# Kernel tuning notes

Hardware: AMD Instinct MI355X
Metric: run time of the kernel (lower is better)

## Reference

```python
import jax, jax.numpy as jnp
import numpy as np

EPS = 1e-5


def conv2d(x, w, b, stride=1, pad=1):
    out = jax.lax.conv_general_dilated(
        x, w, (stride, stride), [(pad, pad), (pad, pad)],
        dimension_numbers=('NCHW', 'OIHW', 'NCHW'))
    return out + b[None, :, None, None]


def bn_inf(x, gamma, beta, mean, var):
    inv = gamma / jnp.sqrt(var + EPS)
    return x * inv[None, :, None, None] + (beta - mean * inv)[None, :, None, None]


def deform_conv(x, offset, weight, stride, pad, dil):
    # x: [B,Ci,H,W], offset: [B,2*K*K,Ho,Wo] (dy,dx interleaved per kernel pos),
    # weight: [Co,Ci,K,K]. torchvision DeformConv2d v1 semantics, no bias.
    B, Ci, H, W = x.shape
    Co, _, K, _ = weight.shape
    KK = K * K
    Ho = (H + 2 * pad - dil * (K - 1) - 1) // stride + 1
    Wo = (W + 2 * pad - dil * (K - 1) - 1) // stride + 1
    dy = offset[:, 0::2]  # [B,KK,Ho,Wo]
    dx = offset[:, 1::2]
    ky, kx = jnp.meshgrid(jnp.arange(K), jnp.arange(K), indexing='ij')
    ky = ky.reshape(KK).astype(x.dtype)
    kx = kx.reshape(KK).astype(x.dtype)
    base_y = (jnp.arange(Ho) * stride - pad).astype(x.dtype)
    base_x = (jnp.arange(Wo) * stride - pad).astype(x.dtype)
    ys = base_y[None, None, :, None] + (ky * dil)[None, :, None, None] + dy
    xs = base_x[None, None, None, :] + (kx * dil)[None, :, None, None] + dx
    y0 = jnp.floor(ys)
    x0 = jnp.floor(xs)
    fy = ys - y0
    fx = xs - x0

    def gather(img, iy, ix):
        # img: [Ci,H,W]; iy, ix: [KK,Ho,Wo] float integer-valued coords
        valid = (iy >= 0) & (iy < H) & (ix >= 0) & (ix < W)
        iyc = jnp.clip(iy, 0, H - 1).astype(jnp.int32)
        ixc = jnp.clip(ix, 0, W - 1).astype(jnp.int32)
        v = img[:, iyc, ixc]  # [Ci,KK,Ho,Wo]
        return v * valid[None].astype(img.dtype)

    def sample_one(img, y0b, x0b, fyb, fxb):
        w00 = (1 - fyb) * (1 - fxb)
        w01 = (1 - fyb) * fxb
        w10 = fyb * (1 - fxb)
        w11 = fyb * fxb
        s = (gather(img, y0b, x0b) * w00[None]
             + gather(img, y0b, x0b + 1) * w01[None]
             + gather(img, y0b + 1, x0b) * w10[None]
             + gather(img, y0b + 1, x0b + 1) * w11[None])
        return s  # [Ci,KK,Ho,Wo]

    sampled = jax.vmap(sample_one)(x, y0, x0, fy, fx)  # [B,Ci,KK,Ho,Wo]
    return jnp.einsum('oik,bikhw->bohw', weight.reshape(Co, Ci, KK), sampled)


def setup_inputs() -> dict:
    key = jax.random.key(0)
    ks = jax.random.split(key, 16)
    B, C, H, W = 8, 128, 64, 64
    d = dict(
        x=jax.random.normal(ks[0], (B, C, H, W), jnp.float32),
        w_off1=jax.random.normal(ks[1], (18, C, 3, 3), jnp.float32) * 0.01,
        b_off1=jnp.zeros((18,), jnp.float32),
        w_dc1=jax.random.normal(ks[2], (C, C, 3, 3), jnp.float32) * 0.05,
        g1=jnp.ones((C,), jnp.float32),
        beta1=jnp.zeros((C,), jnp.float32),
        m1=jax.random.normal(ks[3], (C,), jnp.float32) * 0.1,
        v1=jax.random.uniform(ks[4], (C,), jnp.float32) + 0.5,
        w_off2=jax.random.normal(ks[5], (18, C, 3, 3), jnp.float32) * 0.01,
        b_off2=jnp.zeros((18,), jnp.float32),
        w_dc2=jax.random.normal(ks[6], (C, C, 3, 3), jnp.float32) * 0.05,
        g2=jnp.ones((C,), jnp.float32),
        beta2=jnp.zeros((C,), jnp.float32),
        m2=jax.random.normal(ks[7], (C,), jnp.float32) * 0.1,
        v2=jax.random.uniform(ks[8], (C,), jnp.float32) + 0.5,
    )
    return d


def reference(x, w_off1, b_off1, w_dc1, g1, beta1, m1, v1,
              w_off2, b_off2, w_dc2, g2, beta2, m2, v2):
    # BasicBlock6 forward (stride=1, in_planes==planes => identity shortcut)
    off1 = conv2d(x, w_off1, b_off1, stride=1, pad=1)
    out = jax.nn.relu(bn_inf(deform_conv(x, off1, w_dc1, 1, 2, 2), g1, beta1, m1, v1))
    off2 = conv2d(out, w_off2, b_off2, stride=1, pad=1)
    out = bn_inf(deform_conv(out, off2, w_dc2, 1, 2, 2), g2, beta2, m2, v2)
    out = out + x  # identity shortcut
    return jax.nn.relu(out)
```

## Files before the change

### kernel.cpp

```cpp
#include <hip/hip_runtime.h>
#include <hip/hip_bf16.h>

#define CH   128
#define HH   64
#define WW   64
#define OFFC 18

typedef __attribute__((ext_vector_type(8))) short bf16x8;
typedef __attribute__((ext_vector_type(4))) short bf16x4;
typedef __attribute__((ext_vector_type(4))) float f32x4;

static __device__ __forceinline__ unsigned short f2bf(float f) {
    __hip_bfloat16 h = __float2bfloat16(f);
    return *reinterpret_cast<unsigned short*>(&h);
}
static __device__ __forceinline__ float bf2f(unsigned short u) {
    union { unsigned int i; float f; } x; x.i = ((unsigned int)u) << 16;
    return x.f;
}

__global__ __launch_bounds__(256) void pack_all_kernel(
    const float* __restrict__ wdc1, const float* __restrict__ wdc2,
    const float* __restrict__ wof1, const float* __restrict__ wof2,
    unsigned short* __restrict__ wpk1, unsigned short* __restrict__ wpk2,
    unsigned short* __restrict__ wpo1, unsigned short* __restrict__ wpo2)
{
    int blk = blockIdx.x;
    int tid = threadIdx.x;
    if (blk < 1152) {
        const float* w = (blk < 576) ? wdc1 : wdc2;
        unsigned short* wp = (blk < 576) ? wpk1 : wpk2;
        int id = (blk % 576) * 256 + tid;
        int j    = id & 7;
        int lane = (id >> 3) & 63;
        int ot   = (id >> 9) & 7;
        int kk   = (id >> 12) & 3;
        int k    = id >> 14;
        int o = ot * 16 + (lane & 15);
        int i = kk * 32 + (lane >> 4) * 8 + j;
        wp[id] = f2bf(w[(o * CH + i) * 9 + k]);
    } else {
        const float* w = (blk < 1296) ? wof1 : wof2;
        unsigned short* wp = (blk < 1296) ? wpo1 : wpo2;
        int id = ((blk - 1152) % 144) * 256 + tid;
        int j    = id & 7;
        int lane = (id >> 3) & 63;
        int mt   = (id >> 9) & 1;
        int kk   = (id >> 10) & 3;
        int k    = id >> 12;
        int o = mt * 16 + (lane & 15);
        int i = kk * 32 + (lane >> 4) * 8 + j;
        wp[id] = (o < OFFC) ? f2bf(w[(o * CH + i) * 9 + k]) : (unsigned short)0;
    }
}

__global__ __launch_bounds__(256) void to_nhwc_kernel(
    const float* __restrict__ x, unsigned short* __restrict__ xh)
{
    __shared__ float s[CH][WW + 1];
    int blk = blockIdx.x;
    int tid = threadIdx.x;
    const float* xb = x + ((size_t)(blk >> 6) * CH * HH + (blk & 63)) * WW;

    int c_off = tid >> 4, w0 = (tid & 15) * 4;
    #pragma unroll
    for (int it = 0; it < 8; ++it) {
        int c = it * 16 + c_off;
        float4 vv = *(const float4*)&xb[(size_t)c * HH * WW + w0];
        s[c][w0] = vv.x; s[c][w0 + 1] = vv.y; s[c][w0 + 2] = vv.z; s[c][w0 + 3] = vv.w;
    }
    __syncthreads();

    int w = tid & 63, c0 = (tid >> 6) * 32;
    unsigned short* dst = xh + ((size_t)blk * WW + w) * CH + c0;
    unsigned short tmp[32];
    #pragma unroll
    for (int j = 0; j < 32; ++j) tmp[j] = f2bf(s[c0 + j][w]);
    #pragma unroll
    for (int q = 0; q < 4; ++q)
        *(bf16x8*)(dst + q * 8) = *(const bf16x8*)(tmp + q * 8);
}

__global__ __launch_bounds__(256) void off_conv_mfma_kernel(
    const unsigned short* __restrict__ xh,
    const unsigned short* __restrict__ wpo,
    const float* __restrict__ bias,
    unsigned short* __restrict__ offh)
{
    int wgid = blockIdx.x;
    int blk  = (wgid & 7) * 64 + (wgid >> 3);
    int b = blk >> 6, oh = blk & 63;
    int tid = threadIdx.x;
    int lane = tid & 63;
    int nt = tid >> 6;
    int nl = lane & 15;
    int kg = lane >> 4;

    f32x4 acc0 = {0.f, 0.f, 0.f, 0.f}, acc1 = {0.f, 0.f, 0.f, 0.f};
    const unsigned short* xb = xh + (size_t)b * HH * WW * CH;

    for (int k = 0; k < 9; ++k) {
        int ky = k / 3, kx = k - ky * 3;
        int ih = oh - 1 + ky;
        if (ih < 0 || ih >= HH) continue;
        int iw = nt * 16 + nl + kx - 1;
        bool valid = (iw >= 0) && (iw < WW);
        const unsigned short* row = xb + ((size_t)ih * WW + (valid ? iw : 0)) * CH + kg * 8;
        const unsigned short* wk = wpo + (size_t)k * 8 * 512;
        #pragma unroll
        for (int kk = 0; kk < 4; ++kk) {
            bf16x8 bfrag = {0, 0, 0, 0, 0, 0, 0, 0};
            if (valid) bfrag = *(const bf16x8*)(row + kk * 32);
            bf16x8 a0 = *(const bf16x8*)(wk + (kk * 2 + 0) * 512 + lane * 8);
            bf16x8 a1 = *(const bf16x8*)(wk + (kk * 2 + 1) * 512 + lane * 8);
            acc0 = __builtin_amdgcn_mfma_f32_16x16x32_bf16(a0, bfrag, acc0, 0, 0, 0);
            acc1 = __builtin_amdgcn_mfma_f32_16x16x32_bf16(a1, bfrag, acc1, 0, 0, 0);
        }
    }

    int ow = nt * 16 + nl;
    #pragma unroll
    for (int r = 0; r < 4; ++r) {
        int co = kg * 4 + r;
        offh[(((size_t)b * OFFC + co) * HH + oh) * WW + ow] = f2bf(acc0[r] + bias[co]);
    }
    if (kg == 0) {
        #pragma unroll
        for (int r = 0; r < 2; ++r) {
            int co = 16 + r;
            offh[(((size_t)b * OFFC + co) * HH + oh) * WW + ow] = f2bf(acc1[r] + bias[co]);
        }
    }
}

__global__ __launch_bounds__(256) void deform_mfma2_kernel(
    const unsigned short* __restrict__ xh,
    const unsigned short* __restrict__ offh,
    const unsigned short* __restrict__ wpk,
    const float* __restrict__ g, const float* __restrict__ beta,
    const float* __restrict__ m, const float* __restrict__ v,
    const float* __restrict__ residual,
    unsigned short* __restrict__ out_h,
    float* __restrict__ out_f)
{
    __shared__ unsigned short sB[32 * 128];

    int wgid = blockIdx.x;
    int blk  = (wgid & 7) * 128 + (wgid >> 3);
    int owh = blk & 1, oh = (blk >> 1) & 63, b = blk >> 7;
    int ow0 = owh * 32;
    int tid = threadIdx.x, lane = tid & 63, wv = tid >> 6;

    int s_ow = tid >> 3;
    int ci0  = (tid & 7) * 16;
    int ow_g = ow0 + s_ow;

    const unsigned short* xb = xh + (size_t)b * HH * WW * CH;

    f32x4 acc[2][2];
    #pragma unroll
    for (int a = 0; a < 2; ++a)
        #pragma unroll
        for (int q = 0; q < 2; ++q) acc[a][q] = (f32x4){0.f, 0.f, 0.f, 0.f};

    for (int k = 0; k < 9; ++k) {
        int ky = k / 3, kx = k - ky * 3;

        float dy = bf2f(offh[(((size_t)b * OFFC + 2 * k) * HH + oh) * WW + ow_g]);
        float dx = bf2f(offh[(((size_t)b * OFFC + 2 * k + 1) * HH + oh) * WW + ow_g]);
        float ys = (float)(oh - 2 + ky * 2) + dy;
        float xs = (float)(ow_g - 2 + kx * 2) + dx;
        float y0f = floorf(ys), x0f = floorf(xs);
        float fy = ys - y0f, fx = xs - x0f;
        int y0 = (int)y0f, x0 = (int)x0f;
        int y1 = y0 + 1,   x1 = x0 + 1;
        bool vy0 = (y0 >= 0) & (y0 < HH);
        bool vy1 = (y1 >= 0) & (y1 < HH);
        bool vx0 = (x0 >= 0) & (x0 < WW);
        bool vx1 = (x1 >= 0) & (x1 < WW);
        int y0c = min(max(y0, 0), HH - 1), y1c = min(max(y1, 0), HH - 1);
        int x0c = min(max(x0, 0), WW - 1), x1c = min(max(x1, 0), WW - 1);
        float cw0 = (1.f - fy) * (1.f - fx) * ((vy0 && vx0) ? 1.f : 0.f);
        float cw1 = (1.f - fy) * fx         * ((vy0 && vx1) ? 1.f : 0.f);
        float cw2 = fy * (1.f - fx)         * ((vy1 && vx0) ? 1.f : 0.f);
        float cw3 = fy * fx                 * ((vy1 && vx1) ? 1.f : 0.f);

        const unsigned short* p0 = xb + ((size_t)(y0c * WW + x0c)) * CH + ci0;
        const unsigned short* p1 = xb + ((size_t)(y0c * WW + x1c)) * CH + ci0;
        const unsigned short* p2 = xb + ((size_t)(y1c * WW + x0c)) * CH + ci0;
        const unsigned short* p3 = xb + ((size_t)(y1c * WW + x1c)) * CH + ci0;

        bf16x8 v00 = *(const bf16x8*)(p0),     v01 = *(const bf16x8*)(p0 + 8);
        bf16x8 v10 = *(const bf16x8*)(p1),     v11 = *(const bf16x8*)(p1 + 8);
        bf16x8 v20 = *(const bf16x8*)(p2),     v21 = *(const bf16x8*)(p2 + 8);
        bf16x8 v30 = *(const bf16x8*)(p3),     v31 = *(const bf16x8*)(p3 + 8);

        union { bf16x8 v8; unsigned short u[8]; } w0, w1;
        #pragma unroll
        for (int j = 0; j < 8; ++j) {
            float a0 = cw0 * bf2f((unsigned short)v00[j])
                     + cw1 * bf2f((unsigned short)v10[j])
                     + cw2 * bf2f((unsigned short)v20[j])
                     + cw3 * bf2f((unsigned short)v30[j]);
            float a1 = cw0 * bf2f((unsigned short)v01[j])
                     + cw1 * bf2f((unsigned short)v11[j])
                     + cw2 * bf2f((unsigned short)v21[j])
                     + cw3 * bf2f((unsigned short)v31[j]);
            w0.u[j] = f2bf(a0);
            w1.u[j] = f2bf(a1);
        }
        int base = s_ow * 256 + ci0 * 2;
        int swz  = (s_ow & 7) << 4;
        *(bf16x8*)((char*)sB + ( base       ^ swz)) = w0.v8;
        *(bf16x8*)((char*)sB + ((base + 16) ^ swz)) = w1.v8;
        __syncthreads();

        const unsigned short* wk = wpk + (size_t)k * 16384;
        #pragma unroll
        for (int kk = 0; kk < 4; ++kk) {
            bf16x8 a0 = *(const bf16x8*)(wk + (kk * 8 + 2 * wv)     * 512 + lane * 8);
            bf16x8 a1 = *(const bf16x8*)(wk + (kk * 8 + 2 * wv + 1) * 512 + lane * 8);
            #pragma unroll
            for (int owt = 0; owt < 2; ++owt) {
                int owl = owt * 16 + (lane & 15);
                int rbyte = (owl * 256 + (kk * 32 + (lane >> 4) * 8) * 2)
                            ^ ((owl & 7) << 4);
                bf16x8 bf = *(const bf16x8*)((const char*)sB + rbyte);
                acc[0][owt] = __builtin_amdgcn_mfma_f32_16x16x32_bf16(
                                  a0, bf, acc[0][owt], 0, 0, 0);
                acc[1][owt] = __builtin_amdgcn_mfma_f32_16x16x32_bf16(
                                  a1, bf, acc[1][owt], 0, 0, 0);
            }
        }
        __syncthreads();
    }

    if (out_h != nullptr) {
        #pragma unroll
        for (int otl = 0; otl < 2; ++otl) {
            int ob = (2 * wv + otl) * 16 + (lane >> 4) * 4;
            float inv[4], sh[4];
            #pragma unroll
            for (int r = 0; r < 4; ++r) {
                int o = ob + r;
                float iv = g[o] / sqrtf(v[o] + 1e-5f);
                inv[r] = iv; sh[r] = beta[o] - m[o] * iv;
            }
            #pragma unroll
            for (int owt = 0; owt < 2; ++owt) {
                int ow = ow0 + owt * 16 + (lane & 15);
                union { bf16x4 v4; unsigned short u[4]; } pk;
                #pragma unroll
                for (int r = 0; r < 4; ++r) {
                    float val = acc[otl][owt][r] * inv[r] + sh[r];
                    pk.u[r] = f2bf(fmaxf(val, 0.f));
                }
                *(bf16x4*)(out_h + ((size_t)(b * HH + oh) * WW + ow) * CH + ob) = pk.v4;
            }
        }
    } else {
        #pragma unroll
        for (int otl = 0; otl < 2; ++otl) {
            #pragma unroll
            for (int r = 0; r < 4; ++r) {
                int o = (2 * wv + otl) * 16 + (lane >> 4) * 4 + r;
                float iv = g[o] / sqrtf(v[o] + 1e-5f);
                float sh = beta[o] - m[o] * iv;
                #pragma unroll
                for (int owt = 0; owt < 2; ++owt) {
                    int ow = ow0 + owt * 16 + (lane & 15);
                    size_t idx = (((size_t)b * CH + o) * HH + oh) * WW + ow;
                    float val = acc[otl][owt][r] * iv + sh + residual[idx];
                    out_f[idx] = fmaxf(val, 0.f);
                }
            }
        }
    }
}

extern "C" void kernel_launch(void* const* d_in, const int* in_sizes, int n_in,
                              void* d_out, int out_size, void* d_ws, size_t ws_size,
                              hipStream_t stream)
{
    const float* x      = (const float*)d_in[0];
    const float* w_off1 = (const float*)d_in[1];
    const float* b_off1 = (const float*)d_in[2];
    const float* w_dc1  = (const float*)d_in[3];
    const float* g1     = (const float*)d_in[4];
    const float* beta1  = (const float*)d_in[5];
    const float* m1     = (const float*)d_in[6];
    const float* v1     = (const float*)d_in[7];
    const float* w_off2 = (const float*)d_in[8];
    const float* b_off2 = (const float*)d_in[9];
    const float* w_dc2  = (const float*)d_in[10];
    const float* g2     = (const float*)d_in[11];
    const float* beta2  = (const float*)d_in[12];
    const float* m2     = (const float*)d_in[13];
    const float* v2     = (const float*)d_in[14];
    float* out = (float*)d_out;

    char* ws = (char*)d_ws;
    unsigned short* xh    = (unsigned short*)ws;
    unsigned short* out1h = (unsigned short*)(ws + 8388608);
    unsigned short* offh  = (unsigned short*)(ws + 16777216);
    unsigned short* wpk1  = (unsigned short*)(ws + 17956864);
    unsigned short* wpk2  = (unsigned short*)(ws + 18251776);
    unsigned short* wpo1  = (unsigned short*)(ws + 18546688);
    unsigned short* wpo2  = (unsigned short*)(ws + 18620416);

    pack_all_kernel<<<1440, 256, 0, stream>>>(w_dc1, w_dc2, w_off1, w_off2,
                                              wpk1, wpk2, wpo1, wpo2);
    to_nhwc_kernel<<<512, 256, 0, stream>>>(x, xh);

    off_conv_mfma_kernel<<<512, 256, 0, stream>>>(xh, wpo1, b_off1, offh);
    deform_mfma2_kernel<<<1024, 256, 0, stream>>>(xh, offh, wpk1,
                                                  g1, beta1, m1, v1,
                                                  nullptr, out1h, nullptr);
    off_conv_mfma_kernel<<<512, 256, 0, stream>>>(out1h, wpo2, b_off2, offh);
    deform_mfma2_kernel<<<1024, 256, 0, stream>>>(out1h, offh, wpk2,
                                                  g2, beta2, m2, v2,
                                                  x, nullptr, out);
}
```

Before: 101.5 us.

## Double-buffer deform sampling with MFMA and merge prep kernels into one launch

The deform kernel now double-buffers its shared-memory sample tile. Gathers for the next kernel tap are issued before the MFMAs for the current tap, so global-load latency can hide behind matrix math. All 18 offsets are loaded up front, and one barrier per tap is removed. The weight-packing and NHWC conversion kernels are merged into a single launch to save launch overhead, at the cost of doubled LDS and higher register pressure in the deform kernel.

```diff
diff --git a/kernel.cpp b/kernel.cpp
--- a/kernel.cpp
+++ b/kernel.cpp
@@ -19,14 +19,17 @@
     return x.f;
 }
 
-__global__ __launch_bounds__(256) void pack_all_kernel(
+__global__ __launch_bounds__(256) void prep_kernel(
+    const float* __restrict__ x, unsigned short* __restrict__ xh,
     const float* __restrict__ wdc1, const float* __restrict__ wdc2,
     const float* __restrict__ wof1, const float* __restrict__ wof2,
     unsigned short* __restrict__ wpk1, unsigned short* __restrict__ wpk2,
     unsigned short* __restrict__ wpo1, unsigned short* __restrict__ wpo2)
 {
+    __shared__ float s[CH][WW + 1];
     int blk = blockIdx.x;
     int tid = threadIdx.x;
+
     if (blk < 1152) {
         const float* w = (blk < 576) ? wdc1 : wdc2;
         unsigned short* wp = (blk < 576) ? wpk1 : wpk2;
@@ -39,7 +42,9 @@
         int o = ot * 16 + (lane & 15);
         int i = kk * 32 + (lane >> 4) * 8 + j;
         wp[id] = f2bf(w[(o * CH + i) * 9 + k]);
-    } else {
+        return;
+    }
+    if (blk < 1440) {
         const float* w = (blk < 1296) ? wof1 : wof2;
         unsigned short* wp = (blk < 1296) ? wpo1 : wpo2;
         int id = ((blk - 1152) % 144) * 256 + tid;
@@ -51,16 +56,11 @@
         int o = mt * 16 + (lane & 15);
         int i = kk * 32 + (lane >> 4) * 8 + j;
         wp[id] = (o < OFFC) ? f2bf(w[(o * CH + i) * 9 + k]) : (unsigned short)0;
-    }
-}
-
-__global__ __launch_bounds__(256) void to_nhwc_kernel(
-    const float* __restrict__ x, unsigned short* __restrict__ xh)
-{
-    __shared__ float s[CH][WW + 1];
-    int blk = blockIdx.x;
-    int tid = threadIdx.x;
-    const float* xb = x + ((size_t)(blk >> 6) * CH * HH + (blk & 63)) * WW;
+        return;
+    }
+
+    int nb = blk - 1440;
+    const float* xb = x + ((size_t)(nb >> 6) * CH * HH + (nb & 63)) * WW;
 
     int c_off = tid >> 4, w0 = (tid & 15) * 4;
     #pragma unroll
@@ -72,7 +72,7 @@
     __syncthreads();
 
     int w = tid & 63, c0 = (tid >> 6) * 32;
-    unsigned short* dst = xh + ((size_t)blk * WW + w) * CH + c0;
+    unsigned short* dst = xh + ((size_t)nb * WW + w) * CH + c0;
     unsigned short tmp[32];
     #pragma unroll
     for (int j = 0; j < 32; ++j) tmp[j] = f2bf(s[c0 + j][w]);
@@ -133,6 +133,75 @@
     }
 }
 
+#define DEF_COORD(K) do {                                                     \
+    int ky = (K) / 3, kx = (K) - ky * 3;                                      \
+    float ys = (float)(oh - 2 + ky * 2) + dyv[K];                             \
+    float xs = (float)(ow_g - 2 + kx * 2) + dxv[K];                           \
+    float y0f = floorf(ys), x0f = floorf(xs);                                 \
+    float fy = ys - y0f, fx = xs - x0f;                                       \
+    int y0 = (int)y0f, x0i = (int)x0f;                                        \
+    int y1 = y0 + 1, x1 = x0i + 1;                                            \
+    bool vy0 = (y0 >= 0) & (y0 < HH), vy1 = (y1 >= 0) & (y1 < HH);            \
+    bool vx0 = (x0i >= 0) & (x0i < WW), vx1 = (x1 >= 0) & (x1 < WW);          \
+    int y0c = min(max(y0, 0), HH - 1), y1c = min(max(y1, 0), HH - 1);         \
+    int x0c = min(max(x0i, 0), WW - 1), x1c = min(max(x1, 0), WW - 1);        \
+    cw0 = (1.f - fy) * (1.f - fx) * ((vy0 && vx0) ? 1.f : 0.f);               \
+    cw1 = (1.f - fy) * fx         * ((vy0 && vx1) ? 1.f : 0.f);               \
+    cw2 = fy * (1.f - fx)         * ((vy1 && vx0) ? 1.f : 0.f);               \
+    cw3 = fy * fx                 * ((vy1 && vx1) ? 1.f : 0.f);               \
+    p0 = xb + ((size_t)(y0c * WW + x0c)) * CH + ci0;                          \
+    p1 = xb + ((size_t)(y0c * WW + x1c)) * CH + ci0;                          \
+    p2 = xb + ((size_t)(y1c * WW + x0c)) * CH + ci0;                          \
+    p3 = xb + ((size_t)(y1c * WW + x1c)) * CH + ci0;                          \
+} while (0)
+
+#define DEF_LOADS() do {                                                      \
+    s0a = *(const bf16x8*)(p0); s0b = *(const bf16x8*)(p0 + 8);               \
+    s1a = *(const bf16x8*)(p1); s1b = *(const bf16x8*)(p1 + 8);               \
+    s2a = *(const bf16x8*)(p2); s2b = *(const bf16x8*)(p2 + 8);               \
+    s3a = *(const bf16x8*)(p3); s3b = *(const bf16x8*)(p3 + 8);               \
+} while (0)
+
+#define DEF_BLEND_WRITE(BUF) do {                                             \
+    union { bf16x8 v8; unsigned short u[8]; } w0u, w1u;                       \
+    _Pragma("unroll")                                                         \
+    for (int j = 0; j < 8; ++j) {                                             \
+        float a0 = cw0 * bf2f((unsigned short)s0a[j])                         \
+                 + cw1 * bf2f((unsigned short)s1a[j])                         \
+                 + cw2 * bf2f((unsigned short)s2a[j])                         \
+                 + cw3 * bf2f((unsigned short)s3a[j]);                        \
+        float a1 = cw0 * bf2f((unsigned short)s0b[j])                         \
+                 + cw1 * bf2f((unsigned short)s1b[j])                         \
+                 + cw2 * bf2f((unsigned short)s2b[j])                         \
+                 + cw3 * bf2f((unsigned short)s3b[j]);                        \
+        w0u.u[j] = f2bf(a0); w1u.u[j] = f2bf(a1);                             \
+    }                                                                         \
+    int base = s_ow * 256 + ci0 * 2;                                          \
+    int swz  = (s_ow & 7) << 4;                                               \
+    *(bf16x8*)((char*)sB[BUF] + ( base        ^ swz)) = w0u.v8;               \
+    *(bf16x8*)((char*)sB[BUF] + ((base + 16)  ^ swz)) = w1u.v8;               \
+} while (0)
+
+#define DEF_MFMA(K, BUF) do {                                                 \
+    const unsigned short* wk = wpk + (size_t)(K) * 16384;                     \
+    _Pragma("unroll")                                                         \
+    for (int kk = 0; kk < 4; ++kk) {                                          \
+        bf16x8 a0 = *(const bf16x8*)(wk + (kk * 8 + 2 * wv)     * 512 + lane * 8); \
+        bf16x8 a1 = *(const bf16x8*)(wk + (kk * 8 + 2 * wv + 1) * 512 + lane * 8); \
+        _Pragma("unroll")                                                     \
+        for (int owt = 0; owt < 2; ++owt) {                                   \
+            int owl = owt * 16 + (lane & 15);                                 \
+            int rbyte = (owl * 256 + (kk * 32 + (lane >> 4) * 8) * 2)         \
+                        ^ ((owl & 7) << 4);                                   \
+            bf16x8 bfv = *(const bf16x8*)((const char*)sB[BUF] + rbyte);      \
+            acc[0][owt] = __builtin_amdgcn_mfma_f32_16x16x32_bf16(            \
+                              a0, bfv, acc[0][owt], 0, 0, 0);                 \
+            acc[1][owt] = __builtin_amdgcn_mfma_f32_16x16x32_bf16(            \
+                              a1, bfv, acc[1][owt], 0, 0, 0);                 \
+        }                                                                     \
+    }                                                                         \
+} while (0)
+
 __global__ __launch_bounds__(256) void deform_mfma2_kernel(
     const unsigned short* __restrict__ xh,
     const unsigned short* __restrict__ offh,
@@ -143,7 +212,7 @@
     unsigned short* __restrict__ out_h,
     float* __restrict__ out_f)
 {
-    __shared__ unsigned short sB[32 * 128];
+    __shared__ unsigned short sB[2][32 * 128];
 
     int wgid = blockIdx.x;
     int blk  = (wgid & 7) * 128 + (wgid >> 3);
@@ -157,81 +226,31 @@
 
     const unsigned short* xb = xh + (size_t)b * HH * WW * CH;
 
+    float dyv[9], dxv[9];
+    #pragma unroll
+    for (int k = 0; k < 9; ++k) {
+        dyv[k] = bf2f(offh[(((size_t)b * OFFC + 2 * k)     * HH + oh) * WW + ow_g]);
+        dxv[k] = bf2f(offh[(((size_t)b * OFFC + 2 * k + 1) * HH + oh) * WW + ow_g]);
+    }
+
     f32x4 acc[2][2];
     #pragma unroll
     for (int a = 0; a < 2; ++a)
         #pragma unroll
         for (int q = 0; q < 2; ++q) acc[a][q] = (f32x4){0.f, 0.f, 0.f, 0.f};
 
+    float cw0, cw1, cw2, cw3;
+    const unsigned short *p0, *p1, *p2, *p3;
+    bf16x8 s0a, s0b, s1a, s1b, s2a, s2b, s3a, s3b;
+
+    DEF_COORD(0); DEF_LOADS(); DEF_BLEND_WRITE(0);
+    __syncthreads();
+
+    #pragma unroll
     for (int k = 0; k < 9; ++k) {
-        int ky = k / 3, kx = k - ky * 3;
-
-        float dy = bf2f(offh[(((size_t)b * OFFC + 2 * k) * HH + oh) * WW + ow_g]);
-        float dx = bf2f(offh[(((size_t)b * OFFC + 2 * k + 1) * HH + oh) * WW + ow_g]);
-        float ys = (float)(oh - 2 + ky * 2) + dy;
-        float xs = (float)(ow_g - 2 + kx * 2) + dx;
-        float y0f = floorf(ys), x0f = floorf(xs);
-        float fy = ys - y0f, fx = xs - x0f;
-        int y0 = (int)y0f, x0 = (int)x0f;
-        int y1 = y0 + 1,   x1 = x0 + 1;
-        bool vy0 = (y0 >= 0) & (y0 < HH);
-        bool vy1 = (y1 >= 0) & (y1 < HH);
-        bool vx0 = (x0 >= 0) & (x0 < WW);
-        bool vx1 = (x1 >= 0) & (x1 < WW);
-        int y0c = min(max(y0, 0), HH - 1), y1c = min(max(y1, 0), HH - 1);
-        int x0c = min(max(x0, 0), WW - 1), x1c = min(max(x1, 0), WW - 1);
-        float cw0 = (1.f - fy) * (1.f - fx) * ((vy0 && vx0) ? 1.f : 0.f);
-        float cw1 = (1.f - fy) * fx         * ((vy0 && vx1) ? 1.f : 0.f);
-        float cw2 = fy * (1.f - fx)         * ((vy1 && vx0) ? 1.f : 0.f);
-        float cw3 = fy * fx                 * ((vy1 && vx1) ? 1.f : 0.f);
-
-        const unsigned short* p0 = xb + ((size_t)(y0c * WW + x0c)) * CH + ci0;
-        const unsigned short* p1 = xb + ((size_t)(y0c * WW + x1c)) * CH + ci0;
-        const unsigned short* p2 = xb + ((size_t)(y1c * WW + x0c)) * CH + ci0;
-        const unsigned short* p3 = xb + ((size_t)(y1c * WW + x1c)) * CH + ci0;
-
-        bf16x8 v00 = *(const bf16x8*)(p0),     v01 = *(const bf16x8*)(p0 + 8);
-        bf16x8 v10 = *(const bf16x8*)(p1),     v11 = *(const bf16x8*)(p1 + 8);
-        bf16x8 v20 = *(const bf16x8*)(p2),     v21 = *(const bf16x8*)(p2 + 8);
-        bf16x8 v30 = *(const bf16x8*)(p3),     v31 = *(const bf16x8*)(p3 + 8);
-
-        union { bf16x8 v8; unsigned short u[8]; } w0, w1;
-        #pragma unroll
-        for (int j = 0; j < 8; ++j) {
-            float a0 = cw0 * bf2f((unsigned short)v00[j])
-                     + cw1 * bf2f((unsigned short)v10[j])
-                     + cw2 * bf2f((unsigned short)v20[j])
-                     + cw3 * bf2f((unsigned short)v30[j]);
-            float a1 = cw0 * bf2f((unsigned short)v01[j])
-                     + cw1 * bf2f((unsigned short)v11[j])
-                     + cw2 * bf2f((unsigned short)v21[j])
-                     + cw3 * bf2f((unsigned short)v31[j]);
-            w0.u[j] = f2bf(a0);
-            w1.u[j] = f2bf(a1);
-        }
-        int base = s_ow * 256 + ci0 * 2;
-        int swz  = (s_ow & 7) << 4;
-        *(bf16x8*)((char*)sB + ( base       ^ swz)) = w0.v8;
-        *(bf16x8*)((char*)sB + ((base + 16) ^ swz)) = w1.v8;
-        __syncthreads();
-
-        const unsigned short* wk = wpk + (size_t)k * 16384;
-        #pragma unroll
-        for (int kk = 0; kk < 4; ++kk) {
-            bf16x8 a0 = *(const bf16x8*)(wk + (kk * 8 + 2 * wv)     * 512 + lane * 8);
-            bf16x8 a1 = *(const bf16x8*)(wk + (kk * 8 + 2 * wv + 1) * 512 + lane * 8);
-            #pragma unroll
-            for (int owt = 0; owt < 2; ++owt) {
-                int owl = owt * 16 + (lane & 15);
-                int rbyte = (owl * 256 + (kk * 32 + (lane >> 4) * 8) * 2)
-                            ^ ((owl & 7) << 4);
-                bf16x8 bf = *(const bf16x8*)((const char*)sB + rbyte);
-                acc[0][owt] = __builtin_amdgcn_mfma_f32_16x16x32_bf16(
-                                  a0, bf, acc[0][owt], 0, 0, 0);
-                acc[1][owt] = __builtin_amdgcn_mfma_f32_16x16x32_bf16(
-                                  a1, bf, acc[1][owt], 0, 0, 0);
-            }
-        }
+        if (k < 8) { DEF_COORD(k + 1); DEF_LOADS(); }
+        DEF_MFMA(k, k & 1);
+        if (k < 8) DEF_BLEND_WRITE((k + 1) & 1);
         __syncthreads();
     }
 
@@ -308,9 +327,8 @@
     unsigned short* wpo1  = (unsigned short*)(ws + 18546688);
     unsigned short* wpo2  = (unsigned short*)(ws + 18620416);
 
-    pack_all_kernel<<<1440, 256, 0, stream>>>(w_dc1, w_dc2, w_off1, w_off2,
-                                              wpk1, wpk2, wpo1, wpo2);
-    to_nhwc_kernel<<<512, 256, 0, stream>>>(x, xh);
+    prep_kernel<<<1952, 256, 0, stream>>>(x, xh, w_dc1, w_dc2, w_off1, w_off2,
+                                          wpk1, wpk2, wpo1, wpo2);
 
     off_conv_mfma_kernel<<<512, 256, 0, stream>>>(xh, wpo1, b_off1, offh);
     deform_mfma2_kernel<<<1024, 256, 0, stream>>>(xh, offh, wpk1,
```

Measured after the change: 102.8 us. No clear change (+1.3%).

## Fuse offset conv into deformable conv kernel and merge prep kernels

Applied to the files above, without the earlier changes.

Computes the 18-channel offset convolution inside the deformable conv block, keeping the offsets in LDS as fp32 instead of writing them to global memory as bf16. Each block now covers a full 64-wide output row instead of half a row, and the weight packing and NHWC conversion are merged into a single prep kernel. This cuts the launch count from six to three and removes the offset buffer round trip. In exchange there are half as many blocks (512), more accumulators per thread, more LDS per block, and a serial offset-conv phase before sampling in each block.

```diff
diff --git a/kernel.cpp b/kernel.cpp
--- a/kernel.cpp
+++ b/kernel.cpp
@@ -19,14 +19,17 @@
     return x.f;
 }
 
-__global__ __launch_bounds__(256) void pack_all_kernel(
+__global__ __launch_bounds__(256) void prep_kernel(
+    const float* __restrict__ x, unsigned short* __restrict__ xh,
     const float* __restrict__ wdc1, const float* __restrict__ wdc2,
     const float* __restrict__ wof1, const float* __restrict__ wof2,
     unsigned short* __restrict__ wpk1, unsigned short* __restrict__ wpk2,
     unsigned short* __restrict__ wpo1, unsigned short* __restrict__ wpo2)
 {
+    __shared__ float s[CH][WW + 1];
     int blk = blockIdx.x;
     int tid = threadIdx.x;
+
     if (blk < 1152) {
         const float* w = (blk < 576) ? wdc1 : wdc2;
         unsigned short* wp = (blk < 576) ? wpk1 : wpk2;
@@ -39,7 +42,9 @@
         int o = ot * 16 + (lane & 15);
         int i = kk * 32 + (lane >> 4) * 8 + j;
         wp[id] = f2bf(w[(o * CH + i) * 9 + k]);
-    } else {
+        return;
+    }
+    if (blk < 1440) {
         const float* w = (blk < 1296) ? wof1 : wof2;
         unsigned short* wp = (blk < 1296) ? wpo1 : wpo2;
         int id = ((blk - 1152) % 144) * 256 + tid;
@@ -51,16 +56,11 @@
         int o = mt * 16 + (lane & 15);
         int i = kk * 32 + (lane >> 4) * 8 + j;
         wp[id] = (o < OFFC) ? f2bf(w[(o * CH + i) * 9 + k]) : (unsigned short)0;
-    }
-}
-
-__global__ __launch_bounds__(256) void to_nhwc_kernel(
-    const float* __restrict__ x, unsigned short* __restrict__ xh)
-{
-    __shared__ float s[CH][WW + 1];
-    int blk = blockIdx.x;
-    int tid = threadIdx.x;
-    const float* xb = x + ((size_t)(blk >> 6) * CH * HH + (blk & 63)) * WW;
+        return;
+    }
+
+    int nb = blk - 1440;
+    const float* xb = x + ((size_t)(nb >> 6) * CH * HH + (nb & 63)) * WW;
 
     int c_off = tid >> 4, w0 = (tid & 15) * 4;
     #pragma unroll
@@ -72,7 +72,7 @@
     __syncthreads();
 
     int w = tid & 63, c0 = (tid >> 6) * 32;
-    unsigned short* dst = xh + ((size_t)blk * WW + w) * CH + c0;
+    unsigned short* dst = xh + ((size_t)nb * WW + w) * CH + c0;
     unsigned short tmp[32];
     #pragma unroll
     for (int j = 0; j < 32; ++j) tmp[j] = f2bf(s[c0 + j][w]);
@@ -81,61 +81,10 @@
         *(bf16x8*)(dst + q * 8) = *(const bf16x8*)(tmp + q * 8);
 }
 
-__global__ __launch_bounds__(256) void off_conv_mfma_kernel(
+__global__ __launch_bounds__(256) void deform_fused_kernel(
     const unsigned short* __restrict__ xh,
     const unsigned short* __restrict__ wpo,
     const float* __restrict__ bias,
-    unsigned short* __restrict__ offh)
-{
-    int wgid = blockIdx.x;
-    int blk  = (wgid & 7) * 64 + (wgid >> 3);
-    int b = blk >> 6, oh = blk & 63;
-    int tid = threadIdx.x;
-    int lane = tid & 63;
-    int nt = tid >> 6;
-    int nl = lane & 15;
-    int kg = lane >> 4;
-
-    f32x4 acc0 = {0.f, 0.f, 0.f, 0.f}, acc1 = {0.f, 0.f, 0.f, 0.f};
-    const unsigned short* xb = xh + (size_t)b * HH * WW * CH;
-
-    for (int k = 0; k < 9; ++k) {
-        int ky = k / 3, kx = k - ky * 3;
-        int ih = oh - 1 + ky;
-        if (ih < 0 || ih >= HH) continue;
-        int iw = nt * 16 + nl + kx - 1;
-        bool valid = (iw >= 0) && (iw < WW);
-        const unsigned short* row = xb + ((size_t)ih * WW + (valid ? iw : 0)) * CH + kg * 8;
-        const unsigned short* wk = wpo + (size_t)k * 8 * 512;
-        #pragma unroll
-        for (int kk = 0; kk < 4; ++kk) {
-            bf16x8 bfrag = {0, 0, 0, 0, 0, 0, 0, 0};
-            if (valid) bfrag = *(const bf16x8*)(row + kk * 32);
-            bf16x8 a0 = *(const bf16x8*)(wk + (kk * 2 + 0) * 512 + lane * 8);
-            bf16x8 a1 = *(const bf16x8*)(wk + (kk * 2 + 1) * 512 + lane * 8);
-            acc0 = __builtin_amdgcn_mfma_f32_16x16x32_bf16(a0, bfrag, acc0, 0, 0, 0);
-            acc1 = __builtin_amdgcn_mfma_f32_16x16x32_bf16(a1, bfrag, acc1, 0, 0, 0);
-        }
-    }
-
-    int ow = nt * 16 + nl;
-    #pragma unroll
-    for (int r = 0; r < 4; ++r) {
-        int co = kg * 4 + r;
-        offh[(((size_t)b * OFFC + co) * HH + oh) * WW + ow] = f2bf(acc0[r] + bias[co]);
-    }
-    if (kg == 0) {
-        #pragma unroll
-        for (int r = 0; r < 2; ++r) {
-            int co = 16 + r;
-            offh[(((size_t)b * OFFC + co) * HH + oh) * WW + ow] = f2bf(acc1[r] + bias[co]);
-        }
-    }
-}
-
-__global__ __launch_bounds__(256) void deform_mfma2_kernel(
-    const unsigned short* __restrict__ xh,
-    const unsigned short* __restrict__ offh,
     const unsigned short* __restrict__ wpk,
     const float* __restrict__ g, const float* __restrict__ beta,
     const float* __restrict__ m, const float* __restrict__ v,
@@ -143,43 +92,77 @@
     unsigned short* __restrict__ out_h,
     float* __restrict__ out_f)
 {
-    __shared__ unsigned short sB[32 * 128];
+    __shared__ unsigned short sB[64 * 128];
+    __shared__ float off_lds[OFFC][WW];
 
     int wgid = blockIdx.x;
-    int blk  = (wgid & 7) * 128 + (wgid >> 3);
-    int owh = blk & 1, oh = (blk >> 1) & 63, b = blk >> 7;
-    int ow0 = owh * 32;
+    int blk  = (wgid & 7) * 64 + (wgid >> 3);
+    int b = blk >> 6, oh = blk & 63;
     int tid = threadIdx.x, lane = tid & 63, wv = tid >> 6;
 
-    int s_ow = tid >> 3;
-    int ci0  = (tid & 7) * 16;
-    int ow_g = ow0 + s_ow;
-
     const unsigned short* xb = xh + (size_t)b * HH * WW * CH;
 
-    f32x4 acc[2][2];
+    {
+        f32x4 oacc0 = {0.f, 0.f, 0.f, 0.f}, oacc1 = {0.f, 0.f, 0.f, 0.f};
+        for (int k = 0; k < 9; ++k) {
+            int ky = k / 3, kx = k - ky * 3;
+            int ih = oh - 1 + ky;
+            if (ih < 0 || ih >= HH) continue;
+            int iw = wv * 16 + (lane & 15) + kx - 1;
+            bool valid = (iw >= 0) && (iw < WW);
+            const unsigned short* row =
+                xb + ((size_t)ih * WW + (valid ? iw : 0)) * CH + (lane >> 4) * 8;
+            const unsigned short* wk = wpo + (size_t)k * 4096;
+            #pragma unroll
+            for (int kk = 0; kk < 4; ++kk) {
+                bf16x8 bfrag = {0, 0, 0, 0, 0, 0, 0, 0};
+                if (valid) bfrag = *(const bf16x8*)(row + kk * 32);
+                bf16x8 a0 = *(const bf16x8*)(wk + (kk * 2 + 0) * 512 + lane * 8);
+                bf16x8 a1 = *(const bf16x8*)(wk + (kk * 2 + 1) * 512 + lane * 8);
+                oacc0 = __builtin_amdgcn_mfma_f32_16x16x32_bf16(a0, bfrag, oacc0, 0, 0, 0);
+                oacc1 = __builtin_amdgcn_mfma_f32_16x16x32_bf16(a1, bfrag, oacc1, 0, 0, 0);
+            }
+        }
+        int ow = wv * 16 + (lane & 15);
+        #pragma unroll
+        for (int r = 0; r < 4; ++r) {
+            int co = (lane >> 4) * 4 + r;
+            off_lds[co][ow] = oacc0[r] + bias[co];
+        }
+        if ((lane >> 4) == 0) {
+            #pragma unroll
+            for (int r = 0; r < 2; ++r) {
+                int co = 16 + r;
+                off_lds[co][ow] = oacc1[r] + bias[co];
+            }
+        }
+    }
+    __syncthreads();
+
+    int s_ow = tid & 63;
+    int ci0  = (tid >> 6) * 32;
+
+    f32x4 acc[2][4];
     #pragma unroll
     for (int a = 0; a < 2; ++a)
         #pragma unroll
-        for (int q = 0; q < 2; ++q) acc[a][q] = (f32x4){0.f, 0.f, 0.f, 0.f};
+        for (int q = 0; q < 4; ++q) acc[a][q] = (f32x4){0.f, 0.f, 0.f, 0.f};
 
     for (int k = 0; k < 9; ++k) {
         int ky = k / 3, kx = k - ky * 3;
 
-        float dy = bf2f(offh[(((size_t)b * OFFC + 2 * k) * HH + oh) * WW + ow_g]);
-        float dx = bf2f(offh[(((size_t)b * OFFC + 2 * k + 1) * HH + oh) * WW + ow_g]);
+        float dy = off_lds[2 * k][s_ow];
+        float dx = off_lds[2 * k + 1][s_ow];
         float ys = (float)(oh - 2 + ky * 2) + dy;
-        float xs = (float)(ow_g - 2 + kx * 2) + dx;
+        float xs = (float)(s_ow - 2 + kx * 2) + dx;
         float y0f = floorf(ys), x0f = floorf(xs);
         float fy = ys - y0f, fx = xs - x0f;
-        int y0 = (int)y0f, x0 = (int)x0f;
-        int y1 = y0 + 1,   x1 = x0 + 1;
-        bool vy0 = (y0 >= 0) & (y0 < HH);
-        bool vy1 = (y1 >= 0) & (y1 < HH);
-        bool vx0 = (x0 >= 0) & (x0 < WW);
-        bool vx1 = (x1 >= 0) & (x1 < WW);
+        int y0 = (int)y0f, x0i = (int)x0f;
+        int y1 = y0 + 1, x1 = x0i + 1;
+        bool vy0 = (y0 >= 0) & (y0 < HH), vy1 = (y1 >= 0) & (y1 < HH);
+        bool vx0 = (x0i >= 0) & (x0i < WW), vx1 = (x1 >= 0) & (x1 < WW);
         int y0c = min(max(y0, 0), HH - 1), y1c = min(max(y1, 0), HH - 1);
-        int x0c = min(max(x0, 0), WW - 1), x1c = min(max(x1, 0), WW - 1);
+        int x0c = min(max(x0i, 0), WW - 1), x1c = min(max(x1, 0), WW - 1);
         float cw0 = (1.f - fy) * (1.f - fx) * ((vy0 && vx0) ? 1.f : 0.f);
         float cw1 = (1.f - fy) * fx         * ((vy0 && vx1) ? 1.f : 0.f);
         float cw2 = fy * (1.f - fx)         * ((vy1 && vx0) ? 1.f : 0.f);
@@ -190,29 +173,30 @@
         const unsigned short* p2 = xb + ((size_t)(y1c * WW + x0c)) * CH + ci0;
         const unsigned short* p3 = xb + ((size_t)(y1c * WW + x1c)) * CH + ci0;
 
-        bf16x8 v00 = *(const bf16x8*)(p0),     v01 = *(const bf16x8*)(p0 + 8);
-        bf16x8 v10 = *(const bf16x8*)(p1),     v11 = *(const bf16x8*)(p1 + 8);
-        bf16x8 v20 = *(const bf16x8*)(p2),     v21 = *(const bf16x8*)(p2 + 8);
-        bf16x8 v30 = *(const bf16x8*)(p3),     v31 = *(const bf16x8*)(p3 + 8);
-
-        union { bf16x8 v8; unsigned short u[8]; } w0, w1;
-        #pragma unroll
-        for (int j = 0; j < 8; ++j) {
-            float a0 = cw0 * bf2f((unsigned short)v00[j])
-                     + cw1 * bf2f((unsigned short)v10[j])
-                     + cw2 * bf2f((unsigned short)v20[j])
-                     + cw3 * bf2f((unsigned short)v30[j]);
-            float a1 = cw0 * bf2f((unsigned short)v01[j])
-                     + cw1 * bf2f((unsigned short)v11[j])
-                     + cw2 * bf2f((unsigned short)v21[j])
-                     + cw3 * bf2f((unsigned short)v31[j]);
-            w0.u[j] = f2bf(a0);
-            w1.u[j] = f2bf(a1);
-        }
         int base = s_ow * 256 + ci0 * 2;
         int swz  = (s_ow & 7) << 4;
-        *(bf16x8*)((char*)sB + ( base       ^ swz)) = w0.v8;
-        *(bf16x8*)((char*)sB + ((base + 16) ^ swz)) = w1.v8;
+        #pragma unroll
+        for (int q = 0; q < 2; ++q) {
+            bf16x8 v0a = *(const bf16x8*)(p0 + q * 16), v0b = *(const bf16x8*)(p0 + q * 16 + 8);
+            bf16x8 v1a = *(const bf16x8*)(p1 + q * 16), v1b = *(const bf16x8*)(p1 + q * 16 + 8);
+            bf16x8 v2a = *(const bf16x8*)(p2 + q * 16), v2b = *(const bf16x8*)(p2 + q * 16 + 8);
+            bf16x8 v3a = *(const bf16x8*)(p3 + q * 16), v3b = *(const bf16x8*)(p3 + q * 16 + 8);
+            union { bf16x8 v8; unsigned short u[8]; } wa, wb;
+            #pragma unroll
+            for (int j = 0; j < 8; ++j) {
+                float a0 = cw0 * bf2f((unsigned short)v0a[j])
+                         + cw1 * bf2f((unsigned short)v1a[j])
+                         + cw2 * bf2f((unsigned short)v2a[j])
+                         + cw3 * bf2f((unsigned short)v3a[j]);
+                float a1 = cw0 * bf2f((unsigned short)v0b[j])
+                         + cw1 * bf2f((unsigned short)v1b[j])
+                         + cw2 * bf2f((unsigned short)v2b[j])
+                         + cw3 * bf2f((unsigned short)v3b[j]);
+                wa.u[j] = f2bf(a0); wb.u[j] = f2bf(a1);
+            }
+            *(bf16x8*)((char*)sB + ((base + q * 32)      ^ swz)) = wa.v8;
+            *(bf16x8*)((char*)sB + ((base + q * 32 + 16) ^ swz)) = wb.v8;
+        }
         __syncthreads();
 
         const unsigned short* wk = wpk + (size_t)k * 16384;
@@ -221,15 +205,15 @@
             bf16x8 a0 = *(const bf16x8*)(wk + (kk * 8 + 2 * wv)     * 512 + lane * 8);
             bf16x8 a1 = *(const bf16x8*)(wk + (kk * 8 + 2 * wv + 1) * 512 + lane * 8);
             #pragma unroll
-            for (int owt = 0; owt < 2; ++owt) {
+            for (int owt = 0; owt < 4; ++owt) {
                 int owl = owt * 16 + (lane & 15);
                 int rbyte = (owl * 256 + (kk * 32 + (lane >> 4) * 8) * 2)
                             ^ ((owl & 7) << 4);
-                bf16x8 bf = *(const bf16x8*)((const char*)sB + rbyte);
+                bf16x8 bfv = *(const bf16x8*)((const char*)sB + rbyte);
                 acc[0][owt] = __builtin_amdgcn_mfma_f32_16x16x32_bf16(
-                                  a0, bf, acc[0][owt], 0, 0, 0);
+                                  a0, bfv, acc[0][owt], 0, 0, 0);
                 acc[1][owt] = __builtin_amdgcn_mfma_f32_16x16x32_bf16(
-                                  a1, bf, acc[1][owt], 0, 0, 0);
+                                  a1, bfv, acc[1][owt], 0, 0, 0);
             }
         }
         __syncthreads();
@@ -247,8 +231,8 @@
                 inv[r] = iv; sh[r] = beta[o] - m[o] * iv;
             }
             #pragma unroll
-            for (int owt = 0; owt < 2; ++owt) {
-                int ow = ow0 + owt * 16 + (lane & 15);
+            for (int owt = 0; owt < 4; ++owt) {
+                int ow = owt * 16 + (lane & 15);
                 union { bf16x4 v4; unsigned short u[4]; } pk;
                 #pragma unroll
                 for (int r = 0; r < 4; ++r) {
@@ -267,8 +251,8 @@
                 float iv = g[o] / sqrtf(v[o] + 1e-5f);
                 float sh = beta[o] - m[o] * iv;
                 #pragma unroll
-                for (int owt = 0; owt < 2; ++owt) {
-                    int ow = ow0 + owt * 16 + (lane & 15);
+                for (int owt = 0; owt < 4; ++owt) {
+                    int ow = owt * 16 + (lane & 15);
                     size_t idx = (((size_t)b * CH + o) * HH + oh) * WW + ow;
                     float val = acc[otl][owt][r] * iv + sh + residual[idx];
                     out_f[idx] = fmaxf(val, 0.f);
@@ -302,22 +286,18 @@
     char* ws = (char*)d_ws;
     unsigned short* xh    = (unsigned short*)ws;
     unsigned short* out1h = (unsigned short*)(ws + 8388608);
-    unsigned short* offh  = (unsigned short*)(ws + 16777216);
-    unsigned short* wpk1  = (unsigned short*)(ws + 17956864);
-    unsigned short* wpk2  = (unsigned short*)(ws + 18251776);
-    unsigned short* wpo1  = (unsigned short*)(ws + 18546688);
-    unsigned short* wpo2  = (unsigned short*)(ws + 18620416);
-
-    pack_all_kernel<<<1440, 256, 0, stream>>>(w_dc1, w_dc2, w_off1, w_off2,
-                                              wpk1, wpk2, wpo1, wpo2);
-    to_nhwc_kernel<<<512, 256, 0, stream>>>(x, xh);
-
-    off_conv_mfma_kernel<<<512, 256, 0, stream>>>(xh, wpo1, b_off1, offh);
-    deform_mfma2_kernel<<<1024, 256, 0, stream>>>(xh, offh, wpk1,
-                                                  g1, beta1, m1, v1,
-                                                  nullptr, out1h, nullptr);
-    off_conv_mfma_kernel<<<512, 256, 0, stream>>>(out1h, wpo2, b_off2, offh);
-    deform_mfma2_kernel<<<1024, 256, 0, stream>>>(out1h, offh, wpk2,
-                                                  g2, beta2, m2, v2,
-                                                  x, nullptr, out);
-}
+    unsigned short* wpk1  = (unsigned short*)(ws + 16777216);
+    unsigned short* wpk2  = (unsigned short*)(ws + 17072128);
+    unsigned short* wpo1  = (unsigned short*)(ws + 17367040);
+    unsigned short* wpo2  = (unsigned short*)(ws + 17440768);
+
+    prep_kernel<<<1952, 256, 0, stream>>>(x, xh, w_dc1, w_dc2, w_off1, w_off2,
+                                          wpk1, wpk2, wpo1, wpo2);
+
+    deform_fused_kernel<<<512, 256, 0, stream>>>(xh, wpo1, b_off1, wpk1,
+                                                 g1, beta1, m1, v1,
+                                                 nullptr, out1h, nullptr);
+    deform_fused_kernel<<<512, 256, 0, stream>>>(out1h, wpo2, b_off2, wpk2,
+                                                 g2, beta2, m2, v2,
+                                                 x, nullptr, out);
+}
```

Result: slower. 127.6 us (+25.7%).

## Build deform-conv MFMA B fragments directly in registers, drop LDS staging

Applied to the files above, without the earlier changes.

The deformable conv kernel now has each wave handle 16 output columns across all 128 output channels. Each lane builds its bilinear-sampled B fragment in registers, so the LDS buffer and the two barriers per kernel position are gone, and the offsets are preloaded once. The grid is halved to one block per output row, with a launch-bounds occupancy hint. The weight-pack and NHWC-transpose kernels are merged into one launch. The cost is more accumulator registers (8 tiles) and weight fragments reloaded per wave from global/L2 rather than shared across waves.

```diff
diff --git a/kernel.cpp b/kernel.cpp
--- a/kernel.cpp
+++ b/kernel.cpp
@@ -19,14 +19,17 @@
     return x.f;
 }
 
-__global__ __launch_bounds__(256) void pack_all_kernel(
+__global__ __launch_bounds__(256) void prep_kernel(
+    const float* __restrict__ x, unsigned short* __restrict__ xh,
     const float* __restrict__ wdc1, const float* __restrict__ wdc2,
     const float* __restrict__ wof1, const float* __restrict__ wof2,
     unsigned short* __restrict__ wpk1, unsigned short* __restrict__ wpk2,
     unsigned short* __restrict__ wpo1, unsigned short* __restrict__ wpo2)
 {
+    __shared__ float s[CH][WW + 1];
     int blk = blockIdx.x;
     int tid = threadIdx.x;
+
     if (blk < 1152) {
         const float* w = (blk < 576) ? wdc1 : wdc2;
         unsigned short* wp = (blk < 576) ? wpk1 : wpk2;
@@ -39,7 +42,9 @@
         int o = ot * 16 + (lane & 15);
         int i = kk * 32 + (lane >> 4) * 8 + j;
         wp[id] = f2bf(w[(o * CH + i) * 9 + k]);
-    } else {
+        return;
+    }
+    if (blk < 1440) {
         const float* w = (blk < 1296) ? wof1 : wof2;
         unsigned short* wp = (blk < 1296) ? wpo1 : wpo2;
         int id = ((blk - 1152) % 144) * 256 + tid;
@@ -51,16 +56,11 @@
         int o = mt * 16 + (lane & 15);
         int i = kk * 32 + (lane >> 4) * 8 + j;
         wp[id] = (o < OFFC) ? f2bf(w[(o * CH + i) * 9 + k]) : (unsigned short)0;
-    }
-}
-
-__global__ __launch_bounds__(256) void to_nhwc_kernel(
-    const float* __restrict__ x, unsigned short* __restrict__ xh)
-{
-    __shared__ float s[CH][WW + 1];
-    int blk = blockIdx.x;
-    int tid = threadIdx.x;
-    const float* xb = x + ((size_t)(blk >> 6) * CH * HH + (blk & 63)) * WW;
+        return;
+    }
+
+    int nb = blk - 1440;
+    const float* xb = x + ((size_t)(nb >> 6) * CH * HH + (nb & 63)) * WW;
 
     int c_off = tid >> 4, w0 = (tid & 15) * 4;
     #pragma unroll
@@ -72,7 +72,7 @@
     __syncthreads();
 
     int w = tid & 63, c0 = (tid >> 6) * 32;
-    unsigned short* dst = xh + ((size_t)blk * WW + w) * CH + c0;
+    unsigned short* dst = xh + ((size_t)nb * WW + w) * CH + c0;
     unsigned short tmp[32];
     #pragma unroll
     for (int j = 0; j < 32; ++j) tmp[j] = f2bf(s[c0 + j][w]);
@@ -106,7 +106,7 @@
         int iw = nt * 16 + nl + kx - 1;
         bool valid = (iw >= 0) && (iw < WW);
         const unsigned short* row = xb + ((size_t)ih * WW + (valid ? iw : 0)) * CH + kg * 8;
-        const unsigned short* wk = wpo + (size_t)k * 8 * 512;
+        const unsigned short* wk = wpo + (size_t)k * 4096;
         #pragma unroll
         for (int kk = 0; kk < 4; ++kk) {
             bf16x8 bfrag = {0, 0, 0, 0, 0, 0, 0, 0};
@@ -133,7 +133,7 @@
     }
 }
 
-__global__ __launch_bounds__(256) void deform_mfma2_kernel(
+__global__ __launch_bounds__(256, 2) void deform_direct_kernel(
     const unsigned short* __restrict__ xh,
     const unsigned short* __restrict__ offh,
     const unsigned short* __restrict__ wpk,
@@ -143,136 +143,103 @@
     unsigned short* __restrict__ out_h,
     float* __restrict__ out_f)
 {
-    __shared__ unsigned short sB[32 * 128];
-
     int wgid = blockIdx.x;
-    int blk  = (wgid & 7) * 128 + (wgid >> 3);
-    int owh = blk & 1, oh = (blk >> 1) & 63, b = blk >> 7;
-    int ow0 = owh * 32;
+    int blk  = (wgid & 7) * 64 + (wgid >> 3);
+    int b = blk >> 6, oh = blk & 63;
     int tid = threadIdx.x, lane = tid & 63, wv = tid >> 6;
 
-    int s_ow = tid >> 3;
-    int ci0  = (tid & 7) * 16;
-    int ow_g = ow0 + s_ow;
+    int ow_g = wv * 16 + (lane & 15);
+    int cig  = lane >> 4;
 
     const unsigned short* xb = xh + (size_t)b * HH * WW * CH;
 
-    f32x4 acc[2][2];
-    #pragma unroll
-    for (int a = 0; a < 2; ++a)
-        #pragma unroll
-        for (int q = 0; q < 2; ++q) acc[a][q] = (f32x4){0.f, 0.f, 0.f, 0.f};
-
+    float dyv[9], dxv[9];
+    #pragma unroll
+    for (int k = 0; k < 9; ++k) {
+        dyv[k] = bf2f(offh[(((size_t)b * OFFC + 2 * k)     * HH + oh) * WW + ow_g]);
+        dxv[k] = bf2f(offh[(((size_t)b * OFFC + 2 * k + 1) * HH + oh) * WW + ow_g]);
+    }
+
+    f32x4 acc[8];
+    #pragma unroll
+    for (int ot = 0; ot < 8; ++ot) acc[ot] = (f32x4){0.f, 0.f, 0.f, 0.f};
+
+    #pragma unroll
     for (int k = 0; k < 9; ++k) {
         int ky = k / 3, kx = k - ky * 3;
 
-        float dy = bf2f(offh[(((size_t)b * OFFC + 2 * k) * HH + oh) * WW + ow_g]);
-        float dx = bf2f(offh[(((size_t)b * OFFC + 2 * k + 1) * HH + oh) * WW + ow_g]);
-        float ys = (float)(oh - 2 + ky * 2) + dy;
-        float xs = (float)(ow_g - 2 + kx * 2) + dx;
+        float ys = (float)(oh - 2 + ky * 2) + dyv[k];
+        float xs = (float)(ow_g - 2 + kx * 2) + dxv[k];
         float y0f = floorf(ys), x0f = floorf(xs);
         float fy = ys - y0f, fx = xs - x0f;
-        int y0 = (int)y0f, x0 = (int)x0f;
-        int y1 = y0 + 1,   x1 = x0 + 1;
-        bool vy0 = (y0 >= 0) & (y0 < HH);
-        bool vy1 = (y1 >= 0) & (y1 < HH);
-        bool vx0 = (x0 >= 0) & (x0 < WW);
-        bool vx1 = (x1 >= 0) & (x1 < WW);
+        int y0 = (int)y0f, x0i = (int)x0f;
+        int y1 = y0 + 1, x1 = x0i + 1;
+        bool vy0 = (y0 >= 0) & (y0 < HH), vy1 = (y1 >= 0) & (y1 < HH);
+        bool vx0 = (x0i >= 0) & (x0i < WW), vx1 = (x1 >= 0) & (x1 < WW);
         int y0c = min(max(y0, 0), HH - 1), y1c = min(max(y1, 0), HH - 1);
-        int x0c = min(max(x0, 0), WW - 1), x1c = min(max(x1, 0), WW - 1);
+        int x0c = min(max(x0i, 0), WW - 1), x1c = min(max(x1, 0), WW - 1);
         float cw0 = (1.f - fy) * (1.f - fx) * ((vy0 && vx0) ? 1.f : 0.f);
         float cw1 = (1.f - fy) * fx         * ((vy0 && vx1) ? 1.f : 0.f);
         float cw2 = fy * (1.f - fx)         * ((vy1 && vx0) ? 1.f : 0.f);
         float cw3 = fy * fx                 * ((vy1 && vx1) ? 1.f : 0.f);
 
-        const unsigned short* p0 = xb + ((size_t)(y0c * WW + x0c)) * CH + ci0;
-        const unsigned short* p1 = xb + ((size_t)(y0c * WW + x1c)) * CH + ci0;
-        const unsigned short* p2 = xb + ((size_t)(y1c * WW + x0c)) * CH + ci0;
-        const unsigned short* p3 = xb + ((size_t)(y1c * WW + x1c)) * CH + ci0;
-
-        bf16x8 v00 = *(const bf16x8*)(p0),     v01 = *(const bf16x8*)(p0 + 8);
-        bf16x8 v10 = *(const bf16x8*)(p1),     v11 = *(const bf16x8*)(p1 + 8);
-        bf16x8 v20 = *(const bf16x8*)(p2),     v21 = *(const bf16x8*)(p2 + 8);
-        bf16x8 v30 = *(const bf16x8*)(p3),     v31 = *(const bf16x8*)(p3 + 8);
-
-        union { bf16x8 v8; unsigned short u[8]; } w0, w1;
-        #pragma unroll
-        for (int j = 0; j < 8; ++j) {
-            float a0 = cw0 * bf2f((unsigned short)v00[j])
-                     + cw1 * bf2f((unsigned short)v10[j])
-                     + cw2 * bf2f((unsigned short)v20[j])
-                     + cw3 * bf2f((unsigned short)v30[j]);
-            float a1 = cw0 * bf2f((unsigned short)v01[j])
-                     + cw1 * bf2f((unsigned short)v11[j])
-                     + cw2 * bf2f((unsigned short)v21[j])
-                     + cw3 * bf2f((unsigned short)v31[j]);
-            w0.u[j] = f2bf(a0);
-            w1.u[j] = f2bf(a1);
-        }
-        int base = s_ow * 256 + ci0 * 2;
-        int swz  = (s_ow & 7) << 4;
-        *(bf16x8*)((char*)sB + ( base       ^ swz)) = w0.v8;
-        *(bf16x8*)((char*)sB + ((base + 16) ^ swz)) = w1.v8;
-        __syncthreads();
+        const unsigned short* p0 = xb + ((size_t)(y0c * WW + x0c)) * CH + cig * 8;
+        const unsigned short* p1 = xb + ((size_t)(y0c * WW + x1c)) * CH + cig * 8;
+        const unsigned short* p2 = xb + ((size_t)(y1c * WW + x0c)) * CH + cig * 8;
+        const unsigned short* p3 = xb + ((size_t)(y1c * WW + x1c)) * CH + cig * 8;
 
         const unsigned short* wk = wpk + (size_t)k * 16384;
+
         #pragma unroll
         for (int kk = 0; kk < 4; ++kk) {
-            bf16x8 a0 = *(const bf16x8*)(wk + (kk * 8 + 2 * wv)     * 512 + lane * 8);
-            bf16x8 a1 = *(const bf16x8*)(wk + (kk * 8 + 2 * wv + 1) * 512 + lane * 8);
-            #pragma unroll
-            for (int owt = 0; owt < 2; ++owt) {
-                int owl = owt * 16 + (lane & 15);
-                int rbyte = (owl * 256 + (kk * 32 + (lane >> 4) * 8) * 2)
-                            ^ ((owl & 7) << 4);
-                bf16x8 bf = *(const bf16x8*)((const char*)sB + rbyte);
-                acc[0][owt] = __builtin_amdgcn_mfma_f32_16x16x32_bf16(
-                                  a0, bf, acc[0][owt], 0, 0, 0);
-                acc[1][owt] = __builtin_amdgcn_mfma_f32_16x16x32_bf16(
-                                  a1, bf, acc[1][owt], 0, 0, 0);
-            }
-        }
-        __syncthreads();
+            bf16x8 g0 = *(const bf16x8*)(p0 + kk * 32);
+            bf16x8 g1 = *(const bf16x8*)(p1 + kk * 32);
+            bf16x8 g2 = *(const bf16x8*)(p2 + kk * 32);
+            bf16x8 g3 = *(const bf16x8*)(p3 + kk * 32);
+
+            union { bf16x8 v8; unsigned short u[8]; } bfr;
+            #pragma unroll
+            for (int j = 0; j < 8; ++j) {
+                float val = cw0 * bf2f((unsigned short)g0[j])
+                          + cw1 * bf2f((unsigned short)g1[j])
+                          + cw2 * bf2f((unsigned short)g2[j])
+                          + cw3 * bf2f((unsigned short)g3[j]);
+                bfr.u[j] = f2bf(val);
+            }
+
+            #pragma unroll
+            for (int ot = 0; ot < 8; ++ot) {
+                bf16x8 a = *(const bf16x8*)(wk + (size_t)(kk * 8 + ot) * 512 + lane * 8);
+                acc[ot] = __builtin_amdgcn_mfma_f32_16x16x32_bf16(a, bfr.v8, acc[ot], 0, 0, 0);
+            }
+        }
     }
 
     if (out_h != nullptr) {
         #pragma unroll
-        for (int otl = 0; otl < 2; ++otl) {
-            int ob = (2 * wv + otl) * 16 + (lane >> 4) * 4;
-            float inv[4], sh[4];
+        for (int ot = 0; ot < 8; ++ot) {
+            int ob = ot * 16 + (lane >> 4) * 4;
+            union { bf16x4 v4; unsigned short u[4]; } pk;
             #pragma unroll
             for (int r = 0; r < 4; ++r) {
                 int o = ob + r;
                 float iv = g[o] / sqrtf(v[o] + 1e-5f);
-                inv[r] = iv; sh[r] = beta[o] - m[o] * iv;
-            }
-            #pragma unroll
-            for (int owt = 0; owt < 2; ++owt) {
-                int ow = ow0 + owt * 16 + (lane & 15);
-                union { bf16x4 v4; unsigned short u[4]; } pk;
-                #pragma unroll
-                for (int r = 0; r < 4; ++r) {
-                    float val = acc[otl][owt][r] * inv[r] + sh[r];
-                    pk.u[r] = f2bf(fmaxf(val, 0.f));
-                }
-                *(bf16x4*)(out_h + ((size_t)(b * HH + oh) * WW + ow) * CH + ob) = pk.v4;
-            }
+                float sh = beta[o] - m[o] * iv;
+                pk.u[r] = f2bf(fmaxf(acc[ot][r] * iv + sh, 0.f));
+            }
+            *(bf16x4*)(out_h + ((size_t)(b * HH + oh) * WW + ow_g) * CH + ob) = pk.v4;
         }
     } else {
         #pragma unroll
-        for (int otl = 0; otl < 2; ++otl) {
+        for (int ot = 0; ot < 8; ++ot) {
             #pragma unroll
             for (int r = 0; r < 4; ++r) {
-                int o = (2 * wv + otl) * 16 + (lane >> 4) * 4 + r;
+                int o = ot * 16 + (lane >> 4) * 4 + r;
                 float iv = g[o] / sqrtf(v[o] + 1e-5f);
                 float sh = beta[o] - m[o] * iv;
-                #pragma unroll
-                for (int owt = 0; owt < 2; ++owt) {
-                    int ow = ow0 + owt * 16 + (lane & 15);
-                    size_t idx = (((size_t)b * CH + o) * HH + oh) * WW + ow;
-                    float val = acc[otl][owt][r] * iv + sh + residual[idx];
-                    out_f[idx] = fmaxf(val, 0.f);
-                }
+                size_t idx = (((size_t)b * CH + o) * HH + oh) * WW + ow_g;
+                float val = acc[ot][r] * iv + sh + residual[idx];
+                out_f[idx] = fmaxf(val, 0.f);
             }
         }
     }
@@ -308,16 +275,15 @@
     unsigned short* wpo1  = (unsigned short*)(ws + 18546688);
     unsigned short* wpo2  = (unsigned short*)(ws + 18620416);
 
-    pack_all_kernel<<<1440, 256, 0, stream>>>(w_dc1, w_dc2, w_off1, w_off2,
-                                              wpk1, wpk2, wpo1, wpo2);
-    to_nhwc_kernel<<<512, 256, 0, stream>>>(x, xh);
+    prep_kernel<<<1952, 256, 0, stream>>>(x, xh, w_dc1, w_dc2, w_off1, w_off2,
+                                          wpk1, wpk2, wpo1, wpo2);
 
     off_conv_mfma_kernel<<<512, 256, 0, stream>>>(xh, wpo1, b_off1, offh);
-    deform_mfma2_kernel<<<1024, 256, 0, stream>>>(xh, offh, wpk1,
+    deform_direct_kernel<<<512, 256, 0, stream>>>(xh, offh, wpk1,
                                                   g1, beta1, m1, v1,
                                                   nullptr, out1h, nullptr);
     off_conv_mfma_kernel<<<512, 256, 0, stream>>>(out1h, wpo2, b_off2, offh);
-    deform_mfma2_kernel<<<1024, 256, 0, stream>>>(out1h, offh, wpk2,
+    deform_direct_kernel<<<512, 256, 0, stream>>>(out1h, offh, wpk2,
                                                   g2, beta2, m2, v2,
                                                   x, nullptr, out);
 }
```

New measurement: 148.8 us. 46.6% more time.
